# Kernel tuning notes

Hardware: AMD Instinct MI355X
Metric: run time of the kernel (lower is better)

Reference implementation:

```python
import jax, jax.numpy as jnp
import numpy as np

N_NODES = 50000
HIDDEN = 128
N_EDGES = 1_600_000


def gcn_conv(x, W, b, src, dst, n_nodes):
    """PyG GCNConv: linear, add self-loops, symmetric deg^-1/2 normalization, scatter-sum."""
    h = x @ W  # [N, D]
    # degree with self-loops: 1 + in-degree from edges (edge weight 1)
    deg = jnp.ones((n_nodes,), h.dtype).at[dst].add(1.0)
    dinv = jax.lax.rsqrt(deg)  # deg^{-1/2}, deg >= 1 so no inf
    # neighbor messages: norm_e = dinv[src] * dinv[dst]
    msgs = h[src] * (dinv[src] * dinv[dst])[:, None]  # [E, D]
    agg = jnp.zeros_like(h).at[dst].add(msgs)
    # self-loop contribution: norm = dinv[i]*dinv[i]
    agg = agg + h * (dinv * dinv)[:, None]
    return agg + b


def setup_inputs() -> dict:
    key = jax.random.key(0)
    ks = jax.random.split(key, 7)
    x = jax.random.normal(ks[0], (N_NODES, HIDDEN), dtype=jnp.float32)
    edge_index = jax.random.randint(ks[1], (2, N_EDGES), 0, N_NODES, dtype=jnp.int64)
    s = 1.0 / np.sqrt(HIDDEN)
    W1 = jax.random.uniform(ks[2], (HIDDEN, HIDDEN), jnp.float32, -s, s)
    b1 = jax.random.uniform(ks[3], (HIDDEN,), jnp.float32, -s, s)
    W2 = jax.random.uniform(ks[4], (HIDDEN, HIDDEN), jnp.float32, -s, s)
    b2 = jax.random.uniform(ks[5], (HIDDEN,), jnp.float32, -s, s)
    return {"x": x, "edge_index": edge_index, "W1": W1, "b1": b1, "W2": W2, "b2": b2}


def reference(x, edge_index, W1, b1, W2, b2):
    src, dst = edge_index[0], edge_index[1]
    h = jax.nn.relu(gcn_conv(x, W1, b1, src, dst, N_NODES))
    z = gcn_conv(h, W2, b2, src, dst, N_NODES)
    return z
```

## Files before the change

### kernel.cpp

```cpp
#include <hip/hip_runtime.h>
#include <hip/hip_fp16.h>
#include <type_traits>

#define D 128


__global__ __launch_bounds__(256) void deg_kernel(const int* __restrict__ dst,
                                                  int* __restrict__ deg,
                                                  int* __restrict__ rank, int E) {
  int e = blockIdx.x * 256 + threadIdx.x;
  if (e >= E) return;
  rank[e] = atomicAdd(&deg[dst[e]], 1);
}


__global__ __launch_bounds__(256) void bsum_kernel(const int* __restrict__ deg,
                                                   int* __restrict__ bsum) {
  __shared__ int ws[4];
  int i0 = blockIdx.x * 1024 + threadIdx.x * 4;
  int4 v = *reinterpret_cast<const int4*>(deg + i0);
  int s = v.x + v.y + v.z + v.w;
  #pragma unroll
  for (int off = 32; off; off >>= 1) s += __shfl_down(s, off);
  if ((threadIdx.x & 63) == 0) ws[threadIdx.x >> 6] = s;
  __syncthreads();
  if (threadIdx.x == 0) bsum[blockIdx.x] = ws[0] + ws[1] + ws[2] + ws[3];
}


__global__ __launch_bounds__(256) void scan_kernel(const int* __restrict__ deg,
                                                   const int* __restrict__ bsum,
                                                   int* __restrict__ offsets,
                                                   float* __restrict__ dinv,
                                                   int N, int E) {
  __shared__ int ts[256];
  int b = blockIdx.x;
  int base = 0;
  for (int t = 0; t < b; ++t) base += bsum[t];

  int i0 = b * 1024 + threadIdx.x * 4;
  int4 v = *reinterpret_cast<const int4*>(deg + i0);
  int t4 = v.x + v.y + v.z + v.w;
  ts[threadIdx.x] = t4;
  __syncthreads();
  #pragma unroll
  for (int off = 1; off < 256; off <<= 1) {
    int u = (threadIdx.x >= off) ? ts[threadIdx.x - off] : 0;
    __syncthreads();
    ts[threadIdx.x] += u;
    __syncthreads();
  }
  int run = base + ts[threadIdx.x] - t4;

  int dd[4] = {v.x, v.y, v.z, v.w};
  #pragma unroll
  for (int k = 0; k < 4; ++k) {
    int i = i0 + k;
    if (i < N) {
      offsets[i] = run;
      dinv[i] = rsqrtf(1.0f + (float)dd[k]);
    }
    run += dd[k];
  }
  if (b == 0 && threadIdx.x == 0) offsets[N] = E;
}


__global__ __launch_bounds__(256) void place_kernel(const int* __restrict__ src,
                                                    const int* __restrict__ dst,
                                                    const int* __restrict__ rank,
                                                    const int* __restrict__ offsets,
                                                    const float* __restrict__ dinv,
                                                    unsigned int* __restrict__ csr, int E) {
  int e = blockIdx.x * 256 + threadIdx.x;
  if (e >= E) return;
  int s = src[e];
  int d = dst[e];
  int pos = offsets[d] + rank[e];
  float nm = dinv[s] * dinv[d];
  unsigned int q = (unsigned int)__float2int_rn(nm * 32767.0f);
  csr[pos] = ((unsigned int)s << 15) | q;
}


template <typename TI>
__global__ __launch_bounds__(256) void gemm_kernel(const TI* __restrict__ X,
                                                   const float* __restrict__ W,
                                                   __half* __restrict__ H, int N) {
  __shared__ float xs[32 * D];
  int row0 = blockIdx.x * 32;
  if constexpr (std::is_same<TI, float>::value) {
    #pragma unroll
    for (int jj = 0; jj < 4; ++jj) {
      int f4 = threadIdx.x + jj * 256;
      int r = f4 >> 5;
      float4 v = make_float4(0.f, 0.f, 0.f, 0.f);
      if (row0 + r < N) v = *reinterpret_cast<const float4*>(X + (size_t)row0 * D + (size_t)f4 * 4);
      *reinterpret_cast<float4*>(xs + f4 * 4) = v;
    }
  } else {
    #pragma unroll
    for (int jj = 0; jj < 2; ++jj) {
      int g8 = threadIdx.x + jj * 256;
      int r = g8 >> 4;
      uint4 raw = make_uint4(0u, 0u, 0u, 0u);
      if (row0 + r < N)
        raw = *reinterpret_cast<const uint4*>((const __half*)X + (size_t)row0 * D + (size_t)g8 * 8);
      const __half2* hp = reinterpret_cast<const __half2*>(&raw);
      float* dst8 = xs + (size_t)g8 * 8;
      #pragma unroll
      for (int k = 0; k < 4; ++k) {
        float2 f = __half22float2(hp[k]);
        dst8[k * 2] = f.x;
        dst8[k * 2 + 1] = f.y;
      }
    }
  }
  __syncthreads();

  int tx = threadIdx.x & 63;
  int ty = threadIdx.x >> 6;
  int c0 = tx * 2;
  float2 acc[8];
  #pragma unroll
  for (int r = 0; r < 8; ++r) acc[r] = make_float2(0.f, 0.f);
  const float* xbase = xs + ty * 8 * D;

  for (int k = 0; k < D; k += 4) {
    float2 w0 = *reinterpret_cast<const float2*>(W + (size_t)(k + 0) * D + c0);
    float2 w1 = *reinterpret_cast<const float2*>(W + (size_t)(k + 1) * D + c0);
    float2 w2 = *reinterpret_cast<const float2*>(W + (size_t)(k + 2) * D + c0);
    float2 w3 = *reinterpret_cast<const float2*>(W + (size_t)(k + 3) * D + c0);
    #pragma unroll
    for (int r = 0; r < 8; ++r) {
      float4 xv = *reinterpret_cast<const float4*>(xbase + r * D + k);
      acc[r].x = fmaf(xv.x, w0.x, acc[r].x); acc[r].y = fmaf(xv.x, w0.y, acc[r].y);
      acc[r].x = fmaf(xv.y, w1.x, acc[r].x); acc[r].y = fmaf(xv.y, w1.y, acc[r].y);
      acc[r].x = fmaf(xv.z, w2.x, acc[r].x); acc[r].y = fmaf(xv.z, w2.y, acc[r].y);
      acc[r].x = fmaf(xv.w, w3.x, acc[r].x); acc[r].y = fmaf(xv.w, w3.y, acc[r].y);
    }
  }

  #pragma unroll
  for (int r = 0; r < 8; ++r) {
    int row = row0 + ty * 8 + r;
    if (row < N)
      *reinterpret_cast<__half2*>(H + (size_t)row * D + c0) = __floats2half2_rn(acc[r].x, acc[r].y);
  }
}


template <int DO_RELU, typename TO>
__global__ __launch_bounds__(256) void agg_kernel(const __half* __restrict__ H,
                                                  const int* __restrict__ offsets,
                                                  const unsigned int* __restrict__ csr,
                                                  const float* __restrict__ dinv,
                                                  const float* __restrict__ bias,
                                                  TO* __restrict__ out, int N) {
  int n = blockIdx.x * 4 + (threadIdx.x >> 6);
  if (n >= N) return;
  int lane = threadIdx.x & 63;
  int g = lane >> 4;
  int l = lane & 15;

  int beg = offsets[n];
  int end = offsets[n + 1];

  float acc[8];
  #pragma unroll
  for (int k = 0; k < 8; ++k) acc[k] = 0.f;

  const __half* Hl = H + l * 8;

  int j = beg + g;
  for (; j + 4 < end; j += 8) {
    unsigned int p0 = csr[j];
    unsigned int p1 = csr[j + 4];
    float m0 = (float)(p0 & 0x7fffu) * (1.0f / 32767.0f);
    float m1 = (float)(p1 & 0x7fffu) * (1.0f / 32767.0f);
    uint4 r0 = *reinterpret_cast<const uint4*>(Hl + (size_t)(p0 >> 15) * D);
    uint4 r1 = *reinterpret_cast<const uint4*>(Hl + (size_t)(p1 >> 15) * D);
    const __half2* h0 = reinterpret_cast<const __half2*>(&r0);
    const __half2* h1 = reinterpret_cast<const __half2*>(&r1);
    #pragma unroll
    for (int k = 0; k < 4; ++k) {
      float2 f0 = __half22float2(h0[k]);
      float2 f1 = __half22float2(h1[k]);
      acc[2 * k]     = fmaf(f0.x, m0, acc[2 * k]);
      acc[2 * k + 1] = fmaf(f0.y, m0, acc[2 * k + 1]);
      acc[2 * k]     = fmaf(f1.x, m1, acc[2 * k]);
      acc[2 * k + 1] = fmaf(f1.y, m1, acc[2 * k + 1]);
    }
  }
  if (j < end) {
    unsigned int p0 = csr[j];
    float m0 = (float)(p0 & 0x7fffu) * (1.0f / 32767.0f);
    uint4 r0 = *reinterpret_cast<const uint4*>(Hl + (size_t)(p0 >> 15) * D);
    const __half2* h0 = reinterpret_cast<const __half2*>(&r0);
    #pragma unroll
    for (int k = 0; k < 4; ++k) {
      float2 f0 = __half22float2(h0[k]);
      acc[2 * k]     = fmaf(f0.x, m0, acc[2 * k]);
      acc[2 * k + 1] = fmaf(f0.y, m0, acc[2 * k + 1]);
    }
  }

  #pragma unroll
  for (int k = 0; k < 8; ++k) {
    acc[k] += __shfl_xor(acc[k], 16);
    acc[k] += __shfl_xor(acc[k], 32);
  }

  if (g == 0) {
    float di = dinv[n];
    float dii = di * di;
    uint4 rs = *reinterpret_cast<const uint4*>(Hl + (size_t)n * D);
    const __half2* hs = reinterpret_cast<const __half2*>(&rs);
    float4 bv0 = *reinterpret_cast<const float4*>(bias + l * 8);
    float4 bv1 = *reinterpret_cast<const float4*>(bias + l * 8 + 4);
    float v[8];
    #pragma unroll
    for (int k = 0; k < 4; ++k) {
      float2 f = __half22float2(hs[k]);
      v[2 * k]     = fmaf(f.x, dii, acc[2 * k]);
      v[2 * k + 1] = fmaf(f.y, dii, acc[2 * k + 1]);
    }
    v[0] += bv0.x; v[1] += bv0.y; v[2] += bv0.z; v[3] += bv0.w;
    v[4] += bv1.x; v[5] += bv1.y; v[6] += bv1.z; v[7] += bv1.w;
    if (DO_RELU) {
      #pragma unroll
      for (int k = 0; k < 8; ++k) v[k] = fmaxf(v[k], 0.f);
    }
    if constexpr (std::is_same<TO, float>::value) {
      float4 o0 = make_float4(v[0], v[1], v[2], v[3]);
      float4 o1 = make_float4(v[4], v[5], v[6], v[7]);
      *reinterpret_cast<float4*>(out + (size_t)n * D + l * 8) = o0;
      *reinterpret_cast<float4*>(out + (size_t)n * D + l * 8 + 4) = o1;
    } else {
      uint4 pk;
      __half2 q0 = __floats2half2_rn(v[0], v[1]);
      __half2 q1 = __floats2half2_rn(v[2], v[3]);
      __half2 q2 = __floats2half2_rn(v[4], v[5]);
      __half2 q3 = __floats2half2_rn(v[6], v[7]);
      pk.x = *reinterpret_cast<unsigned int*>(&q0);
      pk.y = *reinterpret_cast<unsigned int*>(&q1);
      pk.z = *reinterpret_cast<unsigned int*>(&q2);
      pk.w = *reinterpret_cast<unsigned int*>(&q3);
      *reinterpret_cast<uint4*>((__half*)out + (size_t)n * D + l * 8) = pk;
    }
  }
}


extern "C" void kernel_launch(void* const* d_in, const int* in_sizes, int n_in,
                              void* d_out, int out_size, void* d_ws, size_t ws_size,
                              hipStream_t stream) {
  const float* x  = (const float*)d_in[0];
  const int* edge = (const int*)d_in[1];
  const float* W1 = (const float*)d_in[2];
  const float* b1 = (const float*)d_in[3];
  const float* W2 = (const float*)d_in[4];
  const float* b2 = (const float*)d_in[5];
  const int N = in_sizes[0] / D;
  const int E = in_sizes[1] / 2;
  const int* srcp = edge;
  const int* dstp = edge + E;
  float* out = (float*)d_out;

  const int NP = (N + 1023) & ~1023;
  const int SB = NP / 1024;

  auto align = [](size_t v) { return (v + 255) & ~(size_t)255; };
  char* ws = (char*)d_ws;
  size_t o = 0;
  int*   deg     = (int*)(ws + o);             o += align((size_t)NP * 4);
  int*   bsum    = (int*)(ws + o);             o += align((size_t)SB * 4);
  int*   offsets = (int*)(ws + o);             o += align((size_t)(N + 1) * 4);
  int*   rank    = (int*)(ws + o);             o += align((size_t)E * 4);
  float* dinv    = (float*)(ws + o);           o += align((size_t)N * 4);
  unsigned int* csr = (unsigned int*)(ws + o); o += align((size_t)E * 4);
  __half* Hh     = (__half*)(ws + o);          o += align((size_t)N * D * 2);
  __half* h1h    = (__half*)(ws + o);          o += align((size_t)N * D * 2);

  hipMemsetAsync(deg, 0, (size_t)NP * 4, stream);
  deg_kernel<<<(E + 255) / 256, 256, 0, stream>>>(dstp, deg, rank, E);
  bsum_kernel<<<SB, 256, 0, stream>>>(deg, bsum);
  scan_kernel<<<SB, 256, 0, stream>>>(deg, bsum, offsets, dinv, N, E);
  place_kernel<<<(E + 255) / 256, 256, 0, stream>>>(srcp, dstp, rank, offsets, dinv, csr, E);

  int gemm_blocks = (N + 31) / 32;
  int agg_blocks = (N + 3) / 4;

  gemm_kernel<float><<<gemm_blocks, 256, 0, stream>>>(x, W1, Hh, N);
  agg_kernel<1, __half><<<agg_blocks, 256, 0, stream>>>(Hh, offsets, csr, dinv, b1, h1h, N);

  gemm_kernel<__half><<<gemm_blocks, 256, 0, stream>>>(h1h, W2, Hh, N);
  agg_kernel<0, float><<<agg_blocks, 256, 0, stream>>>(Hh, offsets, csr, dinv, b2, out, N);
}
```

Baseline: 282.8 us.

## Bucket CSR neighbors by source chunk to improve gather locality

Builds the CSR using a two-level key (destination node, source chunk of 4096 nodes). Each node's neighbor list therefore comes out roughly sorted by source index, and the aggregation gathers of H rows gain some cache locality across concurrently running nodes. In exchange the scan array grows 13x (650K entries), the serial per-block base loop in scan2 becomes longer with ~635 blocks, and a separate dinv kernel is added.

```diff
diff --git a/kernel.cpp b/kernel.cpp
--- a/kernel.cpp
+++ b/kernel.cpp
@@ -3,22 +3,26 @@
 #include <type_traits>
 
 #define D 128
-
-
-__global__ __launch_bounds__(256) void deg_kernel(const int* __restrict__ dst,
-                                                  int* __restrict__ deg,
-                                                  int* __restrict__ rank, int E) {
+#define NCH 13
+#define CSH 12
+
+
+__global__ __launch_bounds__(256) void deg2_kernel(const int* __restrict__ src,
+                                                   const int* __restrict__ dst,
+                                                   int* __restrict__ deg2,
+                                                   int* __restrict__ rank, int E) {
   int e = blockIdx.x * 256 + threadIdx.x;
   if (e >= E) return;
-  rank[e] = atomicAdd(&deg[dst[e]], 1);
-}
-
-
-__global__ __launch_bounds__(256) void bsum_kernel(const int* __restrict__ deg,
+  int b = dst[e] * NCH + (src[e] >> CSH);
+  rank[e] = atomicAdd(&deg2[b], 1);
+}
+
+
+__global__ __launch_bounds__(256) void bsum_kernel(const int* __restrict__ deg2,
                                                    int* __restrict__ bsum) {
   __shared__ int ws[4];
   int i0 = blockIdx.x * 1024 + threadIdx.x * 4;
-  int4 v = *reinterpret_cast<const int4*>(deg + i0);
+  int4 v = *reinterpret_cast<const int4*>(deg2 + i0);
   int s = v.x + v.y + v.z + v.w;
   #pragma unroll
   for (int off = 32; off; off >>= 1) s += __shfl_down(s, off);
@@ -28,18 +32,17 @@
 }
 
 
-__global__ __launch_bounds__(256) void scan_kernel(const int* __restrict__ deg,
-                                                   const int* __restrict__ bsum,
-                                                   int* __restrict__ offsets,
-                                                   float* __restrict__ dinv,
-                                                   int N, int E) {
+__global__ __launch_bounds__(256) void scan2_kernel(const int* __restrict__ deg2,
+                                                    const int* __restrict__ bsum,
+                                                    int* __restrict__ offsets,
+                                                    int M, int E) {
   __shared__ int ts[256];
   int b = blockIdx.x;
   int base = 0;
   for (int t = 0; t < b; ++t) base += bsum[t];
 
   int i0 = b * 1024 + threadIdx.x * 4;
-  int4 v = *reinterpret_cast<const int4*>(deg + i0);
+  int4 v = *reinterpret_cast<const int4*>(deg2 + i0);
   int t4 = v.x + v.y + v.z + v.w;
   ts[threadIdx.x] = t4;
   __syncthreads();
@@ -56,13 +59,19 @@
   #pragma unroll
   for (int k = 0; k < 4; ++k) {
     int i = i0 + k;
-    if (i < N) {
-      offsets[i] = run;
-      dinv[i] = rsqrtf(1.0f + (float)dd[k]);
-    }
+    if (i < M) offsets[i] = run;
     run += dd[k];
   }
-  if (b == 0 && threadIdx.x == 0) offsets[N] = E;
+  if (b == 0 && threadIdx.x == 0) offsets[M] = E;
+}
+
+
+__global__ __launch_bounds__(256) void dinv_kernel(const int* __restrict__ offsets,
+                                                   float* __restrict__ dinv, int N) {
+  int n = blockIdx.x * 256 + threadIdx.x;
+  if (n >= N) return;
+  int dg = offsets[(n + 1) * NCH] - offsets[n * NCH];
+  dinv[n] = rsqrtf(1.0f + (float)dg);
 }
 
 
@@ -76,7 +85,7 @@
   if (e >= E) return;
   int s = src[e];
   int d = dst[e];
-  int pos = offsets[d] + rank[e];
+  int pos = offsets[d * NCH + (s >> CSH)] + rank[e];
   float nm = dinv[s] * dinv[d];
   unsigned int q = (unsigned int)__float2int_rn(nm * 32767.0f);
   csr[pos] = ((unsigned int)s << 15) | q;
@@ -163,8 +172,8 @@
   int g = lane >> 4;
   int l = lane & 15;
 
-  int beg = offsets[n];
-  int end = offsets[n + 1];
+  int beg = offsets[n * NCH];
+  int end = offsets[(n + 1) * NCH];
 
   float acc[8];
   #pragma unroll
@@ -267,25 +276,27 @@
   const int* dstp = edge + E;
   float* out = (float*)d_out;
 
-  const int NP = (N + 1023) & ~1023;
-  const int SB = NP / 1024;
+  const int M  = N * NCH;
+  const int MP = (M + 1023) & ~1023;
+  const int SB = MP / 1024;
 
   auto align = [](size_t v) { return (v + 255) & ~(size_t)255; };
   char* ws = (char*)d_ws;
   size_t o = 0;
-  int*   deg     = (int*)(ws + o);             o += align((size_t)NP * 4);
+  int*   deg2    = (int*)(ws + o);             o += align((size_t)MP * 4);
   int*   bsum    = (int*)(ws + o);             o += align((size_t)SB * 4);
-  int*   offsets = (int*)(ws + o);             o += align((size_t)(N + 1) * 4);
+  int*   offsets = (int*)(ws + o);             o += align((size_t)(M + 1) * 4);
   int*   rank    = (int*)(ws + o);             o += align((size_t)E * 4);
   float* dinv    = (float*)(ws + o);           o += align((size_t)N * 4);
   unsigned int* csr = (unsigned int*)(ws + o); o += align((size_t)E * 4);
   __half* Hh     = (__half*)(ws + o);          o += align((size_t)N * D * 2);
   __half* h1h    = (__half*)(ws + o);          o += align((size_t)N * D * 2);
 
-  hipMemsetAsync(deg, 0, (size_t)NP * 4, stream);
-  deg_kernel<<<(E + 255) / 256, 256, 0, stream>>>(dstp, deg, rank, E);
-  bsum_kernel<<<SB, 256, 0, stream>>>(deg, bsum);
-  scan_kernel<<<SB, 256, 0, stream>>>(deg, bsum, offsets, dinv, N, E);
+  hipMemsetAsync(deg2, 0, (size_t)MP * 4, stream);
+  deg2_kernel<<<(E + 255) / 256, 256, 0, stream>>>(srcp, dstp, deg2, rank, E);
+  bsum_kernel<<<SB, 256, 0, stream>>>(deg2, bsum);
+  scan2_kernel<<<SB, 256, 0, stream>>>(deg2, bsum, offsets, M, E);
+  dinv_kernel<<<(N + 255) / 256, 256, 0, stream>>>(offsets, dinv, N);
   place_kernel<<<(E + 255) / 256, 256, 0, stream>>>(srcp, dstp, rank, offsets, dinv, csr, E);
 
   int gemm_blocks = (N + 31) / 32;
```

Measured after the change: 298.1 us. 5.4% more time.
